# Kernel tuning notes

Hardware: AMD Instinct MI355X
Metric: run time of the kernel (lower is better)

The kernel has to match this reference:

```python
import jax, jax.numpy as jnp
import numpy as np
from jax import lax

B, IMG, P, D, DEPTH = 32, 512, 16, 256, 8
G = IMG // P            # 32 grid side
N = G * G               # 1024 tokens
DQ = D // 8             # 32 (CCNet-style reduced q/k dim)
DF = 4 * D

# fixed Laplacian kernel for EdgeTokenExtractor (depthwise, HWIO with I=1)
_LAP = np.array([[0., -1., 0.], [-1., 4., -1.], [0., -1., 0.]], np.float32)


def setup_inputs() -> dict:
    key = jax.random.key(0)
    ks = jax.random.split(key, 16)
    s = 0.02
    return {
        'x': jax.random.normal(ks[0], (B, 1, IMG, IMG), jnp.float32),
        'w_patch': jax.random.normal(ks[1], (D, 1, P, P), jnp.float32) * s,
        'b_patch': jnp.zeros((D,), jnp.float32),
        'pos': jax.random.normal(ks[2], (1, N, D), jnp.float32) * s,
        'w_edge': jax.random.normal(ks[3], (D, D), jnp.float32) * s,
        'b_edge': jnp.zeros((D,), jnp.float32),
        'ln_g': jnp.ones((DEPTH, D), jnp.float32),
        'ln_b': jnp.zeros((DEPTH, D), jnp.float32),
        'wq': jax.random.normal(ks[4], (DEPTH, D, DQ), jnp.float32) * s,
        'bq': jnp.zeros((DEPTH, DQ), jnp.float32),
        'wk': jax.random.normal(ks[5], (DEPTH, D, DQ), jnp.float32) * s,
        'bk': jnp.zeros((DEPTH, DQ), jnp.float32),
        'wv': jax.random.normal(ks[6], (DEPTH, D, D), jnp.float32) * s,
        'bv': jnp.zeros((DEPTH, D), jnp.float32),
        'gamma': jnp.full((DEPTH,), 0.1, jnp.float32),
        'w1': jax.random.normal(ks[7], (DEPTH, D, DF), jnp.float32) * s,
        'b1': jnp.zeros((DEPTH, DF), jnp.float32),
        'w2': jax.random.normal(ks[8], (DEPTH, DF, D), jnp.float32) * s,
        'b2': jnp.zeros((DEPTH, D), jnp.float32),
        'w_head': jax.random.normal(ks[9], (D, 1), jnp.float32) * s,
        'b_head': jnp.zeros((1,), jnp.float32),
    }


def _ln(x, g, b):
    m = x.mean(-1, keepdims=True)
    v = ((x - m) ** 2).mean(-1, keepdims=True)
    return (x - m) * lax.rsqrt(v + 1e-5) * g + b


def _criss_cross(xn, wq, bq, wk, bk, wv, bv, gamma):
    # xn: [B,N,D] -> grid [B,G,G,D]; each token attends to its row + column.
    b_ = xn.shape[0]
    grid = xn.reshape(b_, G, G, D)
    q = grid @ wq + bq            # [B,G,G,DQ]
    k = grid @ wk + bk
    v = grid @ wv + bv            # [B,G,G,D]
    scale = 1.0 / np.sqrt(DQ).astype(np.float32)
    row = jnp.einsum('bhwc,bhvc->bhwv', q, k) * scale   # attend along width
    col = jnp.einsum('bhwc,buwc->bhwu', q, k) * scale   # attend along height
    # mask the duplicated self position in the column branch (CCNet trick)
    col = col - 1e9 * jnp.eye(G, dtype=col.dtype)[:, None, :]
    a = jax.nn.softmax(jnp.concatenate([row, col], axis=-1), axis=-1)  # [B,G,G,2G]
    out = (jnp.einsum('bhwv,bhvc->bhwc', a[..., :G], v)
           + jnp.einsum('bhwu,buwc->bhwc', a[..., G:], v))
    return (gamma * out + grid).reshape(b_, N, D)


def _edge_tokens(t, w_edge, b_edge):
    # depthwise Laplacian over the token grid, then linear + tanh
    b_ = t.shape[0]
    grid = t.reshape(b_, G, G, D)
    kern = jnp.tile(jnp.asarray(_LAP).reshape(3, 3, 1, 1), (1, 1, 1, D))  # [3,3,1,D]
    e = lax.conv_general_dilated(grid, kern, (1, 1), 'SAME',
                                 dimension_numbers=('NHWC', 'HWIO', 'NHWC'),
                                 feature_group_count=D)
    return jnp.tanh(e.reshape(b_, N, D) @ w_edge + b_edge)


def reference(x, w_patch, b_patch, pos, w_edge, b_edge, ln_g, ln_b,
              wq, bq, wk, bk, wv, bv, gamma, w1, b1, w2, b2, w_head, b_head):
    b_ = x.shape[0]
    # patch embed: conv stride=patch -> [B,D,G,G] -> [B,N,D]
    t = lax.conv_general_dilated(x, w_patch, (P, P), 'VALID',
                                 dimension_numbers=('NCHW', 'OIHW', 'NCHW'))
    t = t + b_patch[None, :, None, None]
    t = t.reshape(b_, D, N).transpose(0, 2, 1)
    t = t + pos
    t = t + _edge_tokens(t, w_edge, b_edge)

    def block(h, p):
        lg, lb, wq_, bq_, wk_, bk_, wv_, bv_, gm, w1_, b1_, w2_, b2_ = p
        # NOTE: original block reuses the SAME LayerNorm params for both sublayers
        h = h + _criss_cross(_ln(h, lg, lb), wq_, bq_, wk_, bk_, wv_, bv_, gm)
        hn = _ln(h, lg, lb)
        h = h + jax.nn.gelu(hn @ w1_ + b1_, approximate=False) @ w2_ + b2_
        return h, None

    t, _ = lax.scan(block, t, (ln_g, ln_b, wq, bq, wk, bk, wv, bv, gamma, w1, b1, w2, b2))
    out = t @ w_head + b_head                      # [B,N,1]
    return out.transpose(0, 2, 1).reshape(b_, 1, G, G)
```

## Files before the change

### kernel.cpp

```cpp
#include <hip/hip_runtime.h>
#include <hip/hip_bf16.h>

#define BB   32
#define IMG  512
#define PP   16
#define DD   256
#define GG   32
#define NN   1024
#define DQ_  32
#define DF_  1024
#define DEPTH_ 8

using short8  = __attribute__((ext_vector_type(8))) short;
using floatx4 = __attribute__((ext_vector_type(4))) float;

__device__ __forceinline__ float bu2f(unsigned short u) {
    return __uint_as_float(((unsigned int)u) << 16);
}
__device__ __forceinline__ unsigned short f2b(float f) {
    unsigned int u = __float_as_uint(f);
    u += 0x7fffu + ((u >> 16) & 1u);
    return (unsigned short)(u >> 16);
}
__device__ __forceinline__ unsigned int pack2(float a, float b) {
    return (unsigned int)f2b(a) | ((unsigned int)f2b(b) << 16);
}
__device__ __forceinline__ float gelu_exact(float x) {
    return 0.5f * x * (1.0f + erff(x * 0.70710678118654752440f));
}
__device__ __forceinline__ float lo16(unsigned int u) {
    return __uint_as_float(u << 16);
}
__device__ __forceinline__ float hi16(unsigned int u) {
    return __uint_as_float(u & 0xffff0000u);
}
__device__ __forceinline__ float dot8(uint4 a, uint4 b) {
    const unsigned int* pa = (const unsigned int*)&a;
    const unsigned int* pb = (const unsigned int*)&b;
    float s = 0.f;
    #pragma unroll
    for (int i = 0; i < 4; ++i)
        s += lo16(pa[i]) * lo16(pb[i]) + hi16(pa[i]) * hi16(pb[i]);
    return s;
}
__device__ __forceinline__ void gld16(unsigned short* lds, const unsigned short* g) {
    __builtin_amdgcn_global_load_lds(
        (const __attribute__((address_space(1))) void*)g,
        (__attribute__((address_space(3))) void*)lds, 16, 0, 0);
}

__global__ __launch_bounds__(256) void k_wtrans(const float* __restrict__ in,
                                                unsigned short* __restrict__ out,
                                                int R, int C) {
    __shared__ float tile[32][33];
    const int l = blockIdx.z;
    const int r0 = blockIdx.x * 32, c0 = blockIdx.y * 32;
    const int tx = threadIdx.x & 31, ty = threadIdx.x >> 5;
    const float* src = in + (size_t)l * R * C;
    unsigned short* dst = out + (size_t)l * R * C;
    #pragma unroll
    for (int i = 0; i < 4; ++i)
        tile[ty + i * 8][tx] = src[(size_t)(r0 + ty + i * 8) * C + c0 + tx];
    __syncthreads();
    #pragma unroll
    for (int i = 0; i < 4; ++i)
        dst[(size_t)(c0 + ty + i * 8) * R + r0 + tx] = f2b(tile[tx][ty + i * 8]);
}

__global__ __launch_bounds__(256) void k_qktrans(const float* __restrict__ wq,
                                                 const float* __restrict__ wk,
                                                 unsigned short* __restrict__ o) {
    const int l = blockIdx.z, j = blockIdx.x, k = threadIdx.x;
    float v = (j < 32) ? wq[(size_t)l * 8192 + k * 32 + j]
                       : wk[(size_t)l * 8192 + k * 32 + (j - 32)];
    o[((size_t)l * 64 + j) * 256 + k] = f2b(v);
}

__global__ void k_bqk(const float* __restrict__ bq, const float* __restrict__ bk,
                      float* __restrict__ o) {
    const int l = blockIdx.x, j = threadIdx.x;
    o[l * 64 + j] = (j < 32) ? bq[l * 32 + j] : bk[l * 32 + (j - 32)];
}

__global__ __launch_bounds__(256) void k_cvt(const float* __restrict__ in,
                                             unsigned short* __restrict__ out) {
    int i = blockIdx.x * 256 + threadIdx.x;
    out[i] = f2b(in[i]);
}

__global__ __launch_bounds__(256) void k_im2col(const float* __restrict__ x,
                                                unsigned short* __restrict__ xp) {
    const int tok = blockIdx.x;
    const int b  = tok >> 10;
    const int n  = tok & (NN - 1);
    const int gi = n >> 5, gj = n & 31;
    const int pi = threadIdx.x >> 4, pj = threadIdx.x & 15;
    xp[(size_t)tok * 256 + threadIdx.x] =
        f2b(x[(size_t)(b * IMG + gi * PP + pi) * IMG + gj * PP + pj]);
}

template <int K, int N, int MODE>
__global__ __launch_bounds__(256) void k_gemm(
    const unsigned short* __restrict__ A, const unsigned short* __restrict__ Bt,
    const float* __restrict__ bias, unsigned short* __restrict__ Cb,
    float* __restrict__ Cf, const float* __restrict__ pos) {
    __shared__ alignas(16) unsigned short As[64 * 32];
    __shared__ alignas(16) unsigned short Bs[64 * 32];
    const int t  = threadIdx.x;
    const int m0 = blockIdx.x * 64, n0 = blockIdx.y * 64;
    const int row = t >> 2, ch = t & 3;
    const unsigned short* ga = A  + (size_t)(m0 + row) * K + ch * 8;
    const unsigned short* gb = Bt + (size_t)(n0 + row) * K + ch * 8;
    const int lane = t & 63, wid = t >> 6;
    const int quad = lane >> 4, r = lane & 15;
    const int wm = (wid >> 1) * 32, wn = (wid & 1) * 32;
    floatx4 acc00 = {0,0,0,0}, acc01 = {0,0,0,0}, acc10 = {0,0,0,0}, acc11 = {0,0,0,0};
    uint4 ra = *(const uint4*)ga;
    uint4 rb = *(const uint4*)gb;
    const int KS = K / 32;
    for (int ks = 0; ks < KS; ++ks) {
        __syncthreads();
        *(uint4*)&As[t * 8] = ra;
        *(uint4*)&Bs[t * 8] = rb;
        __syncthreads();
        if (ks + 1 < KS) {
            ra = *(const uint4*)(ga + (ks + 1) * 32);
            rb = *(const uint4*)(gb + (ks + 1) * 32);
        }
        short8 a0 = *(const short8*)&As[(wm + r) * 32 + quad * 8];
        short8 a1 = *(const short8*)&As[(wm + 16 + r) * 32 + quad * 8];
        short8 b0 = *(const short8*)&Bs[(wn + r) * 32 + quad * 8];
        short8 b1 = *(const short8*)&Bs[(wn + 16 + r) * 32 + quad * 8];
        acc00 = __builtin_amdgcn_mfma_f32_16x16x32_bf16(a0, b0, acc00, 0, 0, 0);
        acc01 = __builtin_amdgcn_mfma_f32_16x16x32_bf16(a0, b1, acc01, 0, 0, 0);
        acc10 = __builtin_amdgcn_mfma_f32_16x16x32_bf16(a1, b0, acc10, 0, 0, 0);
        acc11 = __builtin_amdgcn_mfma_f32_16x16x32_bf16(a1, b1, acc11, 0, 0, 0);
    }
    const int nA = n0 + wn + r;
    const int nB = nA + 16;
    const float bias0 = bias[nA], bias1 = bias[nB];
    #pragma unroll
    for (int i = 0; i < 2; ++i) {
        floatx4 aj0 = i ? acc10 : acc00;
        floatx4 aj1 = i ? acc11 : acc01;
        const int mb = m0 + wm + i * 16 + quad * 4;
        #pragma unroll
        for (int g = 0; g < 4; ++g) {
            const int m = mb + g;
            float v0 = aj0[g] + bias0, v1 = aj1[g] + bias1;
            if (MODE == 2) {
                Cb[(size_t)m * N + nA] = f2b(v0);
                Cb[(size_t)m * N + nB] = f2b(v1);
            }
        }
    }
}

template <int K, int N, int MODE>
__global__ __launch_bounds__(256) void k_gemm128(
    const unsigned short* __restrict__ A, const unsigned short* __restrict__ Bt,
    const float* __restrict__ bias, unsigned short* __restrict__ Cb,
    float* __restrict__ Cf, const float* __restrict__ pos) {
    __shared__ alignas(16) unsigned short As[128 * 32];
    __shared__ alignas(16) unsigned short Bs[128 * 32];
    const int t  = threadIdx.x;
    const int m0 = blockIdx.x * 128, n0 = blockIdx.y * 128;
    const int row = t >> 2, ch = t & 3;
    const unsigned short* gA0 = A  + (size_t)(m0 + row) * K + ch * 8;
    const unsigned short* gA1 = A  + (size_t)(m0 + 64 + row) * K + ch * 8;
    const unsigned short* gB0 = Bt + (size_t)(n0 + row) * K + ch * 8;
    const unsigned short* gB1 = Bt + (size_t)(n0 + 64 + row) * K + ch * 8;

    const int lane = t & 63, wid = t >> 6;
    const int quad = lane >> 4, r = lane & 15;
    const int wm = (wid >> 1) * 64, wn = (wid & 1) * 64;

    floatx4 acc[4][4];
    #pragma unroll
    for (int i = 0; i < 4; ++i)
        #pragma unroll
        for (int n = 0; n < 4; ++n) acc[i][n] = floatx4{0.f, 0.f, 0.f, 0.f};

    const int KS = K / 32;
    for (int ks = 0; ks < KS; ++ks) {
        __syncthreads();
        gld16(&As[t * 8],        gA0 + ks * 32);
        gld16(&As[2048 + t * 8], gA1 + ks * 32);
        gld16(&Bs[t * 8],        gB0 + ks * 32);
        gld16(&Bs[2048 + t * 8], gB1 + ks * 32);
        __syncthreads();
        short8 a[4], b[4];
        #pragma unroll
        for (int i = 0; i < 4; ++i)
            a[i] = *(const short8*)&As[(wm + i * 16 + r) * 32 + quad * 8];
        #pragma unroll
        for (int n = 0; n < 4; ++n)
            b[n] = *(const short8*)&Bs[(wn + n * 16 + r) * 32 + quad * 8];
        #pragma unroll
        for (int i = 0; i < 4; ++i)
            #pragma unroll
            for (int n = 0; n < 4; ++n)
                acc[i][n] = __builtin_amdgcn_mfma_f32_16x16x32_bf16(
                    a[i], b[n], acc[i][n], 0, 0, 0);
    }
    #pragma unroll
    for (int n = 0; n < 4; ++n) {
        const int col = n0 + wn + n * 16 + r;
        const float bs = bias[col];
        #pragma unroll
        for (int i = 0; i < 4; ++i) {
            const int mb = m0 + wm + i * 16 + quad * 4;
            #pragma unroll
            for (int g = 0; g < 4; ++g) {
                const int m = mb + g;
                float v0 = acc[i][n][g] + bs;
                if (MODE == 0)      Cb[(size_t)m * N + col] = f2b(gelu_exact(v0));
                else if (MODE == 1) Cf[(size_t)m * N + col] += v0;
                else if (MODE == 2) Cb[(size_t)m * N + col] = f2b(v0);
                else if (MODE == 3) Cf[(size_t)m * N + col] += tanhf(v0);
                else Cf[(size_t)m * N + col] =
                         v0 + pos[(size_t)(m & (NN - 1)) * N + col];
            }
        }
    }
}

__global__ __launch_bounds__(256) void k_lap(const float* __restrict__ h,
                                             unsigned short* __restrict__ e) {
    int idx = blockIdx.x * 256 + threadIdx.x;
    int n  = (idx >> 8) & (NN - 1);
    int gi = n >> 5, gj = n & 31;
    float c  = h[idx];
    float up = (gi > 0)  ? h[idx - GG * DD] : 0.f;
    float dn = (gi < 31) ? h[idx + GG * DD] : 0.f;
    float lf = (gj > 0)  ? h[idx - DD] : 0.f;
    float rt = (gj < 31) ? h[idx + DD] : 0.f;
    e[idx] = f2b(4.f * c - up - dn - lf - rt);
}

__global__ __launch_bounds__(256) void k_ln(
    const float* __restrict__ h, const float* __restrict__ g,
    const float* __restrict__ b, unsigned short* __restrict__ xnb, int layer) {
    const int wid = threadIdx.x >> 6, lane = threadIdx.x & 63;
    const int row = blockIdx.x * 4 + wid;
    const float4 xv = *(const float4*)(h + (size_t)row * DD + lane * 4);
    float s = xv.x + xv.y + xv.z + xv.w;
    #pragma unroll
    for (int o = 32; o; o >>= 1) s += __shfl_xor(s, o, 64);
    const float m = s * (1.f / 256.f);
    float t0 = xv.x - m, t1 = xv.y - m, t2 = xv.z - m, t3 = xv.w - m;
    float s2 = t0 * t0 + t1 * t1 + t2 * t2 + t3 * t3;
    #pragma unroll
    for (int o = 32; o; o >>= 1) s2 += __shfl_xor(s2, o, 64);
    const float r = rsqrtf(s2 * (1.f / 256.f) + 1e-5f);
    const int d0 = lane * 4;
    const float4 gv = *(const float4*)(g + layer * DD + d0);
    const float4 bv = *(const float4*)(b + layer * DD + d0);
    uint2 outp;
    outp.x = pack2(t0 * r * gv.x + bv.x, t1 * r * gv.y + bv.y);
    outp.y = pack2(t2 * r * gv.z + bv.z, t3 * r * gv.w + bv.w);
    *(uint2*)(xnb + (size_t)row * DD + d0) = outp;
}

__global__ __launch_bounds__(256) void k_score(
    const unsigned short* __restrict__ qkb, unsigned short* __restrict__ P) {
    const int wid = threadIdx.x >> 6, lane = threadIdx.x & 63;
    const int tok = blockIdx.x * 4 + wid;
    const int b = tok >> 10, n = tok & (NN - 1);
    const int gi = n >> 5, gj = n & 31;
    const uint4* qp = (const uint4*)(qkb + (size_t)tok * 64);
    uint4 q0 = qp[0], q1 = qp[1], q2 = qp[2], q3 = qp[3];
    const int key = (lane < 32) ? (b * NN + gi * 32 + lane)
                                : (b * NN + (lane - 32) * 32 + gj);
    const uint4* kp = (const uint4*)(qkb + (size_t)key * 64 + 32);
    uint4 k0 = kp[0], k1 = kp[1], k2 = kp[2], k3 = kp[3];
    float s = dot8(q0, k0) + dot8(q1, k1) + dot8(q2, k2) + dot8(q3, k3);
    s *= 0.17677669529663687f;
    if (lane >= 32 && (lane - 32) == gi) s -= 1e9f;
    float m = s;
    #pragma unroll
    for (int o = 32; o; o >>= 1) m = fmaxf(m, __shfl_xor(m, o, 64));
    float e = expf(s - m);
    float sum = e;
    #pragma unroll
    for (int o = 32; o; o >>= 1) sum += __shfl_xor(sum, o, 64);
    P[(size_t)tok * 64 + lane] = f2b(e / sum);
}

__global__ __launch_bounds__(256) void k_avcol(
    const unsigned short* __restrict__ P, const unsigned short* __restrict__ v,
    float* __restrict__ h, const float* __restrict__ gamma, int layer) {
    const int idx = blockIdx.x;
    const int b = idx >> 7, gj = (idx >> 2) & 31, oct = idx & 3;
    const int wid = threadIdx.x >> 6, lane = threadIdx.x & 63;
    const int d0 = lane * 4;
    uint2 vr[32];
    const unsigned short* vbase = v + ((size_t)(b * NN + gj)) * 256 + d0;
    #pragma unroll
    for (int u = 0; u < 32; ++u)
        vr[u] = *(const uint2*)(vbase + (size_t)u * 32 * 256);
    const float g = gamma[layer];
    size_t hidx[2];
    float4 hv[2];
    unsigned int pa[2][16];
    #pragma unroll
    for (int jj = 0; jj < 2; ++jj) {
        const int gi = oct * 8 + wid * 2 + jj;
        const int tok = b * NN + gi * 32 + gj;
        hidx[jj] = (size_t)tok * 256 + d0;
        const uint4* pp = (const uint4*)(P + (size_t)tok * 64 + 32);
        *(uint4*)(pa[jj])      = pp[0];
        *(uint4*)(pa[jj] + 4)  = pp[1];
        *(uint4*)(pa[jj] + 8)  = pp[2];
        *(uint4*)(pa[jj] + 12) = pp[3];
        hv[jj] = *(const float4*)(h + hidx[jj]);
    }
    #pragma unroll
    for (int jj = 0; jj < 2; ++jj) {
        float o0 = 0.f, o1 = 0.f, o2 = 0.f, o3 = 0.f;
        #pragma unroll
        for (int u = 0; u < 32; ++u) {
            float p = (u & 1) ? hi16(pa[jj][u >> 1]) : lo16(pa[jj][u >> 1]);
            o0 += p * lo16(vr[u].x); o1 += p * hi16(vr[u].x);
            o2 += p * lo16(vr[u].y); o3 += p * hi16(vr[u].y);
        }
        float4 r = hv[jj];
        r.x += g * o0; r.y += g * o1; r.z += g * o2; r.w += g * o3;
        *(float4*)(h + hidx[jj]) = r;
    }
}

__global__ __launch_bounds__(256) void k_avrow_ln(
    const unsigned short* __restrict__ P, const unsigned short* __restrict__ v,
    float* __restrict__ h, unsigned short* __restrict__ xnb,
    const float* __restrict__ gamma, const float* __restrict__ lg,
    const float* __restrict__ lb, int layer) {
    const int idx = blockIdx.x;
    const int b = idx >> 7, gi = (idx >> 2) & 31, oct = idx & 3;
    const int wid = threadIdx.x >> 6, lane = threadIdx.x & 63;
    const int d0 = lane * 4;
    uint2 vr[32];
    const unsigned short* vbase = v + ((size_t)(b * NN + gi * 32)) * 256 + d0;
    #pragma unroll
    for (int w = 0; w < 32; ++w)
        vr[w] = *(const uint2*)(vbase + (size_t)w * 256);
    const float g = gamma[layer];
    const float4 gv = *(const float4*)(lg + layer * DD + d0);
    const float4 bv = *(const float4*)(lb + layer * DD + d0);
    size_t hidx[2];
    float4 hv[2];
    uint2 xu[2];
    unsigned int pa[2][16];
    #pragma unroll
    for (int jj = 0; jj < 2; ++jj) {
        const int gj = oct * 8 + wid * 2 + jj;
        const int tok = b * NN + gi * 32 + gj;
        hidx[jj] = (size_t)tok * 256 + d0;
        const uint4* pp = (const uint4*)(P + (size_t)tok * 64);
        *(uint4*)(pa[jj])      = pp[0];
        *(uint4*)(pa[jj] + 4)  = pp[1];
        *(uint4*)(pa[jj] + 8)  = pp[2];
        *(uint4*)(pa[jj] + 12) = pp[3];
        hv[jj] = *(const float4*)(h + hidx[jj]);
        xu[jj] = *(const uint2*)(xnb + hidx[jj]);
    }
    #pragma unroll
    for (int jj = 0; jj < 2; ++jj) {
        float o0 = 0.f, o1 = 0.f, o2 = 0.f, o3 = 0.f;
        #pragma unroll
        for (int w = 0; w < 32; ++w) {
            float p = (w & 1) ? hi16(pa[jj][w >> 1]) : lo16(pa[jj][w >> 1]);
            o0 += p * lo16(vr[w].x); o1 += p * hi16(vr[w].x);
            o2 += p * lo16(vr[w].y); o3 += p * hi16(vr[w].y);
        }
        float f0 = hv[jj].x + lo16(xu[jj].x) + g * o0;
        float f1 = hv[jj].y + hi16(xu[jj].x) + g * o1;
        float f2 = hv[jj].z + lo16(xu[jj].y) + g * o2;
        float f3 = hv[jj].w + hi16(xu[jj].y) + g * o3;
        float s = f0 + f1 + f2 + f3;
        #pragma unroll
        for (int o = 32; o; o >>= 1) s += __shfl_xor(s, o, 64);
        const float m = s * (1.f / 256.f);
        float t0 = f0 - m, t1 = f1 - m, t2 = f2 - m, t3 = f3 - m;
        float s2 = t0 * t0 + t1 * t1 + t2 * t2 + t3 * t3;
        #pragma unroll
        for (int o = 32; o; o >>= 1) s2 += __shfl_xor(s2, o, 64);
        const float r = rsqrtf(s2 * (1.f / 256.f) + 1e-5f);
        float4 hvout = {f0, f1, f2, f3};
        *(float4*)(h + hidx[jj]) = hvout;
        uint2 outp;
        outp.x = pack2(t0 * r * gv.x + bv.x, t1 * r * gv.y + bv.y);
        outp.y = pack2(t2 * r * gv.z + bv.z, t3 * r * gv.w + bv.w);
        *(uint2*)(xnb + hidx[jj]) = outp;
    }
}

__global__ __launch_bounds__(256) void k_head(
    const float* __restrict__ h, const float* __restrict__ wh,
    const float* __restrict__ bh, float* __restrict__ out) {
    const int tok  = blockIdx.x * 4 + (threadIdx.x >> 6);
    const int lane = threadIdx.x & 63;
    float acc = 0.f;
    #pragma unroll
    for (int i = 0; i < 4; ++i)
        acc += h[(size_t)tok * DD + lane + 64 * i] * wh[lane + 64 * i];
    #pragma unroll
    for (int o = 32; o; o >>= 1) acc += __shfl_down(acc, o, 64);
    if (lane == 0) out[tok] = acc + bh[0];
}

extern "C" void kernel_launch(void* const* d_in, const int* in_sizes, int n_in,
                              void* d_out, int out_size, void* d_ws, size_t ws_size,
                              hipStream_t stream) {
    const float* fx   = (const float*)d_in[0];
    const float* fwp  = (const float*)d_in[1];
    const float* fbp  = (const float*)d_in[2];
    const float* fpos = (const float*)d_in[3];
    const float* fwe  = (const float*)d_in[4];
    const float* fbe  = (const float*)d_in[5];
    const float* flg  = (const float*)d_in[6];
    const float* flb  = (const float*)d_in[7];
    const float* fwq  = (const float*)d_in[8];
    const float* fbq  = (const float*)d_in[9];
    const float* fwk  = (const float*)d_in[10];
    const float* fbk  = (const float*)d_in[11];
    const float* fwv  = (const float*)d_in[12];
    const float* fbv  = (const float*)d_in[13];
    const float* fgam = (const float*)d_in[14];
    const float* fw1  = (const float*)d_in[15];
    const float* fb1  = (const float*)d_in[16];
    const float* fw2  = (const float*)d_in[17];
    const float* fb2  = (const float*)d_in[18];
    const float* fwh  = (const float*)d_in[19];
    const float* fbh  = (const float*)d_in[20];
    float* out = (float*)d_out;

    float* ws = (float*)d_ws;
    float*          h    = ws;
    unsigned short* xnb  = (unsigned short*)(ws + 8388608);
    unsigned short* w1t  = (unsigned short*)(ws + 12582912);
    unsigned short* w2t  = (unsigned short*)(ws + 13631488);
    unsigned short* wvT  = (unsigned short*)(ws + 14680064);
    unsigned short* wqkT = (unsigned short*)(ws + 14942208);
    unsigned short* wpb  = (unsigned short*)(ws + 15007744);
    unsigned short* weT  = (unsigned short*)(ws + 15040512);
    float*          bqk  = ws + 15073280;
    float* S = ws + 15073792;
    unsigned short* qkb  = (unsigned short*)S;
    unsigned short* v    = (unsigned short*)(S + 1048576);
    unsigned short* P    = (unsigned short*)(S + 5242880);
    unsigned short* xp   = (unsigned short*)S;
    unsigned short* e    = (unsigned short*)S;
    unsigned short* Hc   = (unsigned short*)S;

    const int TOK = BB * NN;

    k_wtrans<<<dim3(8, 32, 8), 256, 0, stream>>>(fw1, w1t, 256, 1024);
    k_wtrans<<<dim3(32, 8, 8), 256, 0, stream>>>(fw2, w2t, 1024, 256);
    k_wtrans<<<dim3(8, 8, 8),  256, 0, stream>>>(fwv, wvT, 256, 256);
    k_wtrans<<<dim3(8, 8, 1),  256, 0, stream>>>(fwe, weT, 256, 256);
    k_qktrans<<<dim3(64, 1, 8), 256, 0, stream>>>(fwq, fwk, wqkT);
    k_bqk<<<8, 64, 0, stream>>>(fbq, fbk, bqk);
    k_cvt<<<256, 256, 0, stream>>>(fwp, wpb);

    k_im2col<<<TOK, 256, 0, stream>>>(fx, xp);
    k_gemm128<256, 256, 4><<<dim3(256, 2), 256, 0, stream>>>(
        xp, wpb, fbp, nullptr, h, fpos);
    k_lap<<<TOK, 256, 0, stream>>>(h, e);
    k_gemm128<256, 256, 3><<<dim3(256, 2), 256, 0, stream>>>(
        e, weT, fbe, nullptr, h, nullptr);

    for (int l = 0; l < DEPTH_; ++l) {
        k_ln<<<TOK / 4, 256, 0, stream>>>(h, flg, flb, xnb, l);
        k_gemm<256, 64, 2><<<dim3(512, 1), 256, 0, stream>>>(
            xnb, wqkT + (size_t)l * 16384, bqk + l * 64, qkb, nullptr, nullptr);
        k_gemm128<256, 256, 2><<<dim3(256, 2), 256, 0, stream>>>(
            xnb, wvT + (size_t)l * 65536, fbv + l * 256, v, nullptr, nullptr);
        k_score<<<TOK / 4, 256, 0, stream>>>(qkb, P);
        k_avcol<<<4096, 256, 0, stream>>>(P, v, h, fgam, l);
        k_avrow_ln<<<4096, 256, 0, stream>>>(P, v, h, xnb, fgam, flg, flb, l);
        for (int c = 0; c < 2; ++c) {
            k_gemm128<256, 1024, 0><<<dim3(128, 8), 256, 0, stream>>>(
                xnb + (size_t)c * 16384 * 256, w1t + (size_t)l * 262144,
                fb1 + (size_t)l * 1024, Hc, nullptr, nullptr);
            k_gemm128<1024, 256, 1><<<dim3(128, 2), 256, 0, stream>>>(
                Hc, w2t + (size_t)l * 262144,
                fb2 + (size_t)l * 256, nullptr, h + (size_t)c * 16384 * 256, nullptr);
        }
    }

    k_head<<<TOK / 4, 256, 0, stream>>>(h, fwh, fbh, out);
}
```

Measured before the change: 1.961 ms.

## Register-prefetch GEMM tiles and use tanh-approximate GELU

Replaces the direct global-to-LDS loads in the 128x128 GEMM with register double-buffering: the next K-slice is loaded into registers while MFMAs run on the current LDS tile, and each thread now handles two 16-byte chunks of one row. It also swaps the exact erf GELU for a tanh-approximation built on __expf to cut epilogue math, and trims unused parameters from the small GEMM. The GELU change alters numerics relative to the exact-GELU reference, and the register prefetch raises register pressure.

```diff
diff --git a/kernel.cpp b/kernel.cpp
--- a/kernel.cpp
+++ b/kernel.cpp
@@ -25,8 +25,10 @@
 __device__ __forceinline__ unsigned int pack2(float a, float b) {
     return (unsigned int)f2b(a) | ((unsigned int)f2b(b) << 16);
 }
-__device__ __forceinline__ float gelu_exact(float x) {
-    return 0.5f * x * (1.0f + erff(x * 0.70710678118654752440f));
+__device__ __forceinline__ float gelu_fast(float x) {
+    float u = 0.7978845608028654f * (x + 0.044715f * x * x * x);
+    float t = 1.f - 2.f / (1.f + __expf(2.f * u));
+    return 0.5f * x * (1.0f + t);
 }
 __device__ __forceinline__ float lo16(unsigned int u) {
     return __uint_as_float(u << 16);
@@ -42,11 +44,6 @@
     for (int i = 0; i < 4; ++i)
         s += lo16(pa[i]) * lo16(pb[i]) + hi16(pa[i]) * hi16(pb[i]);
     return s;
-}
-__device__ __forceinline__ void gld16(unsigned short* lds, const unsigned short* g) {
-    __builtin_amdgcn_global_load_lds(
-        (const __attribute__((address_space(1))) void*)g,
-        (__attribute__((address_space(3))) void*)lds, 16, 0, 0);
 }
 
 __global__ __launch_bounds__(256) void k_wtrans(const float* __restrict__ in,
@@ -102,8 +99,7 @@
 template <int K, int N, int MODE>
 __global__ __launch_bounds__(256) void k_gemm(
     const unsigned short* __restrict__ A, const unsigned short* __restrict__ Bt,
-    const float* __restrict__ bias, unsigned short* __restrict__ Cb,
-    float* __restrict__ Cf, const float* __restrict__ pos) {
+    const float* __restrict__ bias, unsigned short* __restrict__ Cb) {
     __shared__ alignas(16) unsigned short As[64 * 32];
     __shared__ alignas(16) unsigned short Bs[64 * 32];
     const int t  = threadIdx.x;
@@ -147,17 +143,14 @@
         #pragma unroll
         for (int g = 0; g < 4; ++g) {
             const int m = mb + g;
-            float v0 = aj0[g] + bias0, v1 = aj1[g] + bias1;
-            if (MODE == 2) {
-                Cb[(size_t)m * N + nA] = f2b(v0);
-                Cb[(size_t)m * N + nB] = f2b(v1);
-            }
+            Cb[(size_t)m * N + nA] = f2b(aj0[g] + bias0);
+            Cb[(size_t)m * N + nB] = f2b(aj1[g] + bias1);
         }
     }
 }
 
 template <int K, int N, int MODE>
-__global__ __launch_bounds__(256) void k_gemm128(
+__global__ __launch_bounds__(256) void k_gemm128r(
     const unsigned short* __restrict__ A, const unsigned short* __restrict__ Bt,
     const float* __restrict__ bias, unsigned short* __restrict__ Cb,
     float* __restrict__ Cf, const float* __restrict__ pos) {
@@ -165,11 +158,9 @@
     __shared__ alignas(16) unsigned short Bs[128 * 32];
     const int t  = threadIdx.x;
     const int m0 = blockIdx.x * 128, n0 = blockIdx.y * 128;
-    const int row = t >> 2, ch = t & 3;
-    const unsigned short* gA0 = A  + (size_t)(m0 + row) * K + ch * 8;
-    const unsigned short* gA1 = A  + (size_t)(m0 + 64 + row) * K + ch * 8;
-    const unsigned short* gB0 = Bt + (size_t)(n0 + row) * K + ch * 8;
-    const unsigned short* gB1 = Bt + (size_t)(n0 + 64 + row) * K + ch * 8;
+    const int srow = t >> 1, sh = (t & 1) * 16;
+    const unsigned short* ga = A  + (size_t)(m0 + srow) * K + sh;
+    const unsigned short* gb = Bt + (size_t)(n0 + srow) * K + sh;
 
     const int lane = t & 63, wid = t >> 6;
     const int quad = lane >> 4, r = lane & 15;
@@ -181,14 +172,24 @@
         #pragma unroll
         for (int n = 0; n < 4; ++n) acc[i][n] = floatx4{0.f, 0.f, 0.f, 0.f};
 
+    uint4 ra0 = *(const uint4*)(ga);
+    uint4 ra1 = *(const uint4*)(ga + 8);
+    uint4 rb0 = *(const uint4*)(gb);
+    uint4 rb1 = *(const uint4*)(gb + 8);
     const int KS = K / 32;
     for (int ks = 0; ks < KS; ++ks) {
         __syncthreads();
-        gld16(&As[t * 8],        gA0 + ks * 32);
-        gld16(&As[2048 + t * 8], gA1 + ks * 32);
-        gld16(&Bs[t * 8],        gB0 + ks * 32);
-        gld16(&Bs[2048 + t * 8], gB1 + ks * 32);
+        *(uint4*)&As[srow * 32 + sh]     = ra0;
+        *(uint4*)&As[srow * 32 + sh + 8] = ra1;
+        *(uint4*)&Bs[srow * 32 + sh]     = rb0;
+        *(uint4*)&Bs[srow * 32 + sh + 8] = rb1;
         __syncthreads();
+        if (ks + 1 < KS) {
+            ra0 = *(const uint4*)(ga + (ks + 1) * 32);
+            ra1 = *(const uint4*)(ga + (ks + 1) * 32 + 8);
+            rb0 = *(const uint4*)(gb + (ks + 1) * 32);
+            rb1 = *(const uint4*)(gb + (ks + 1) * 32 + 8);
+        }
         short8 a[4], b[4];
         #pragma unroll
         for (int i = 0; i < 4; ++i)
@@ -214,7 +215,7 @@
             for (int g = 0; g < 4; ++g) {
                 const int m = mb + g;
                 float v0 = acc[i][n][g] + bs;
-                if (MODE == 0)      Cb[(size_t)m * N + col] = f2b(gelu_exact(v0));
+                if (MODE == 0)      Cb[(size_t)m * N + col] = f2b(gelu_fast(v0));
                 else if (MODE == 1) Cf[(size_t)m * N + col] += v0;
                 else if (MODE == 2) Cb[(size_t)m * N + col] = f2b(v0);
                 else if (MODE == 3) Cf[(size_t)m * N + col] += tanhf(v0);
@@ -464,26 +465,26 @@
     k_cvt<<<256, 256, 0, stream>>>(fwp, wpb);
 
     k_im2col<<<TOK, 256, 0, stream>>>(fx, xp);
-    k_gemm128<256, 256, 4><<<dim3(256, 2), 256, 0, stream>>>(
+    k_gemm128r<256, 256, 4><<<dim3(256, 2), 256, 0, stream>>>(
         xp, wpb, fbp, nullptr, h, fpos);
     k_lap<<<TOK, 256, 0, stream>>>(h, e);
-    k_gemm128<256, 256, 3><<<dim3(256, 2), 256, 0, stream>>>(
+    k_gemm128r<256, 256, 3><<<dim3(256, 2), 256, 0, stream>>>(
         e, weT, fbe, nullptr, h, nullptr);
 
     for (int l = 0; l < DEPTH_; ++l) {
         k_ln<<<TOK / 4, 256, 0, stream>>>(h, flg, flb, xnb, l);
         k_gemm<256, 64, 2><<<dim3(512, 1), 256, 0, stream>>>(
-            xnb, wqkT + (size_t)l * 16384, bqk + l * 64, qkb, nullptr, nullptr);
-        k_gemm128<256, 256, 2><<<dim3(256, 2), 256, 0, stream>>>(
+            xnb, wqkT + (size_t)l * 16384, bqk + l * 64, qkb);
+        k_gemm128r<256, 256, 2><<<dim3(256, 2), 256, 0, stream>>>(
             xnb, wvT + (size_t)l * 65536, fbv + l * 256, v, nullptr, nullptr);
         k_score<<<TOK / 4, 256, 0, stream>>>(qkb, P);
         k_avcol<<<4096, 256, 0, stream>>>(P, v, h, fgam, l);
         k_avrow_ln<<<4096, 256, 0, stream>>>(P, v, h, xnb, fgam, flg, flb, l);
         for (int c = 0; c < 2; ++c) {
-            k_gemm128<256, 1024, 0><<<dim3(128, 8), 256, 0, stream>>>(
+            k_gemm128r<256, 1024, 0><<<dim3(128, 8), 256, 0, stream>>>(
                 xnb + (size_t)c * 16384 * 256, w1t + (size_t)l * 262144,
                 fb1 + (size_t)l * 1024, Hc, nullptr, nullptr);
-            k_gemm128<1024, 256, 1><<<dim3(128, 2), 256, 0, stream>>>(
+            k_gemm128r<1024, 256, 1><<<dim3(128, 2), 256, 0, stream>>>(
                 Hc, w2t + (size_t)l * 262144,
                 fb2 + (size_t)l * 256, nullptr, h + (size_t)c * 16384 * 256, nullptr);
         }
```

New measurement: 2.078 ms. 1.06x slower.
